# Kernel optimization log

Measured on AMD Instinct MI355X. Metric: run time of the kernel, lower is better.

## Reference

```python
import jax, jax.numpy as jnp
import numpy as np
from functools import partial

K = 64
KERNEL_SIZE = 16
TAU = 10.0
THETA = 0.5
GAMMA = 10.0
ALPHA = float(np.exp(-1.0 / TAU))
BETA = 1.0 - ALPHA

@jax.custom_vjp
def spike(x):
    return (x >= 0).astype(x.dtype)

def _spike_fwd(x):
    return spike(x), x

def _spike_bwd(x, g):
    surrogate = GAMMA * jnp.maximum(1.0 - GAMMA * jnp.abs(x), 0.0)
    return (g * surrogate,)

spike.defvjp(_spike_fwd, _spike_bwd)

def setup_inputs() -> dict:
    key = jax.random.key(0)
    k1, k2 = jax.random.split(key)
    B, T = 256, 4096
    x = jax.random.normal(k1, (B, 1, T), dtype=jnp.float32)
    # conv weight [K, 1, ks], init N(0, 1/sqrt(ks))
    W = jax.random.normal(k2, (K, 1, KERNEL_SIZE), dtype=jnp.float32) / np.sqrt(KERNEL_SIZE)
    return {"x": x, "W": W}

def _forward(x, W):
    B = x.shape[0]
    x = x.reshape(B, 1, -1)  # [B,1,T]
    # causal conv: left pad ks-1 -> output length T
    u = jax.lax.conv_general_dilated(
        x, W,
        window_strides=(1,),
        padding=[(KERNEL_SIZE - 1, 0)],
        dimension_numbers=("NCH", "OIH", "NCH"),
    )  # [B,K,T]
    u_t = jnp.transpose(u, (2, 0, 1))  # [T,B,K]
    v0 = jnp.zeros((B, K), dtype=x.dtype)

    def step(v, ut):
        v = ALPHA * v + BETA * ut                      # leak + input
        s_raw = spike(v - THETA)                        # [B,K]
        winner = jax.lax.stop_gradient(jnp.argmax(v, axis=1))  # [B]
        winner_spiked = jnp.take_along_axis(s_raw, winner[:, None], axis=1)  # [B,1]
        wta_mask = jax.nn.one_hot(winner, K, dtype=s_raw.dtype) * winner_spiked
        s = s_raw * wta_mask
        v = v - s * THETA                               # reset
        return v, s

    _, spikes_t = jax.lax.scan(step, v0, u_t)  # [T,B,K]
    return jnp.transpose(spikes_t, (1, 2, 0))  # [B,K,T]

def reference(x, W):
    return _forward(x, W)
```

## Files before the change

### kernel.cpp

```cpp
#include <hip/hip_runtime.h>

#define T_LEN  4096
#define KS     16
#define NSEG   8
#define SEG_CH 32
#define WARM_CH 24

#define ALPHA_F 0.9048374180359595f
#define BETA_F  0.09516258196404048f
#define THETA_F 0.5f

__device__ __forceinline__ float wave64_max_all(float v) {
  float m, t;
  asm("s_nop 1\n\t"
      "v_max_f32 %0, %2, %2 quad_perm:[1,0,3,2] row_mask:0xf bank_mask:0xf\n\t"
      "s_nop 1\n\t"
      "v_max_f32 %0, %0, %0 quad_perm:[2,3,0,1] row_mask:0xf bank_mask:0xf\n\t"
      "s_nop 1\n\t"
      "v_max_f32 %0, %0, %0 row_half_mirror row_mask:0xf bank_mask:0xf\n\t"
      "s_nop 1\n\t"
      "v_max_f32 %0, %0, %0 row_mirror row_mask:0xf bank_mask:0xf\n\t"
      "v_mov_b32 %1, %0\n\t"
      "s_nop 1\n\t"
      "v_permlane32_swap_b32 %1, %0\n\t"
      "s_nop 1\n\t"
      "v_max_f32 %0, %0, %1\n\t"
      "v_mov_b32 %1, %0\n\t"
      "s_nop 1\n\t"
      "v_permlane16_swap_b32 %1, %0\n\t"
      "s_nop 1\n\t"
      "v_max_f32 %0, %0, %1"
      : "=&v"(m), "=&v"(t)
      : "v"(v));
  return m;
}

__global__ __launch_bounds__(128, 4)
void convlif_wta_kernel(const float* __restrict__ x, const float* __restrict__ W,
                        float* __restrict__ out) {
  const int blk  = blockIdx.x;
  const int b    = blk >> 3;
  const int seg  = blk & (NSEG - 1);
  const int wave = threadIdx.x >> 6;
  const int lane = threadIdx.x & 63;

  const int cout0  = seg * SEG_CH;
  const int cstart = (cout0 > WARM_CH) ? (cout0 - WARM_CH) : 0;
  const int cend   = cout0 + SEG_CH;
  const int nch    = cend - cstart;

  __shared__ float vbuf[2][64];

  float w[KS];
  {
    const float4* w4 = reinterpret_cast<const float4*>(W + lane * KS);
    #pragma unroll
    for (int q = 0; q < 4; ++q) {
      float4 a = w4[q];
      w[4*q+0] = a.x; w[4*q+1] = a.y; w[4*q+2] = a.z; w[4*q+3] = a.w;
    }
  }

  const float4* xv4 = reinterpret_cast<const float4*>(x + (size_t)b * T_LEN);
  float* orow = out + ((size_t)(b * 64 + lane)) * T_LEN;

  float u[16];

  auto conv_chunk = [&](int c) {
    float xf[32];
    if (c == 0) {
      #pragma unroll
      for (int m = 0; m < 16; ++m) xf[m] = 0.0f;
    } else {
      const int b4 = 4 * c - 4;
      #pragma unroll
      for (int q = 0; q < 4; ++q) {
        float4 a = xv4[b4 + q];
        xf[4*q+0] = a.x; xf[4*q+1] = a.y; xf[4*q+2] = a.z; xf[4*q+3] = a.w;
      }
    }
    #pragma unroll
    for (int q = 0; q < 4; ++q) {
      float4 a = xv4[4*c + q];
      xf[16+4*q+0] = a.x; xf[16+4*q+1] = a.y;
      xf[16+4*q+2] = a.z; xf[16+4*q+3] = a.w;
    }
    #pragma unroll
    for (int i = 0; i < 16; ++i) {
      float acc = w[0] * xf[1 + i];
      #pragma unroll
      for (int j = 1; j < KS; ++j) acc = fmaf(w[j], xf[1 + i + j], acc);
      u[i] = BETA_F * acc;
    }
  };

  if (wave == 0) conv_chunk(cstart);

  for (int s = 0; s < nch; ++s) {
    const int c = cstart + s;
    if ((s & 1) == wave) {
      float v = (s == 0) ? 0.0f : vbuf[(s - 1) & 1][lane];
      float sv[16];
      #pragma unroll
      for (int i = 0; i < 16; ++i) {
        float vr = fmaf(ALPHA_F, v, u[i]);
        float vm = vr - THETA_F;
        unsigned long long sp = __ballot(vr >= THETA_F);
        bool c1 = (vr >= THETA_F);
        sv[i] = c1 ? 1.0f : 0.0f;
        v     = c1 ? vm : vr;
        if (__builtin_expect((sp & (sp - 1ull)) != 0ull, 0)) {
          float m = wave64_max_all(vr);
          unsigned long long eq = __ballot(vr == m);
          bool win = (lane == __builtin_ctzll(eq));
          sv[i] = win ? 1.0f : 0.0f;
          v     = win ? vm : vr;
        }
      }
      vbuf[s & 1][lane] = v;

      if (c >= cout0) {
        float4* p = reinterpret_cast<float4*>(orow + (size_t)c * 16);
        p[0] = make_float4(sv[0],  sv[1],  sv[2],  sv[3]);
        p[1] = make_float4(sv[4],  sv[5],  sv[6],  sv[7]);
        p[2] = make_float4(sv[8],  sv[9],  sv[10], sv[11]);
        p[3] = make_float4(sv[12], sv[13], sv[14], sv[15]);
      }
    } else {
      if (c + 1 < cend) conv_chunk(c + 1);
    }
    __syncthreads();
  }
}

extern "C" void kernel_launch(void* const* d_in, const int* in_sizes, int n_in,
                              void* d_out, int out_size, void* d_ws, size_t ws_size,
                              hipStream_t stream) {
  const float* x   = (const float*)d_in[0];
  const float* W   = (const float*)d_in[1];
  float*       out = (float*)d_out;
  convlif_wta_kernel<<<dim3(256 * NSEG), dim3(128), 0, stream>>>(x, W, out);
}
```

Before: 115.3 us.

## Split conv producer across two waves in a rotating three-wave pipeline

```diff
diff --git a/kernel.cpp b/kernel.cpp
--- a/kernel.cpp
+++ b/kernel.cpp
@@ -35,7 +35,7 @@
   return m;
 }
 
-__global__ __launch_bounds__(128, 4)
+__global__ __launch_bounds__(192, 6)
 void convlif_wta_kernel(const float* __restrict__ x, const float* __restrict__ W,
                         float* __restrict__ out) {
   const int blk  = blockIdx.x;
@@ -49,6 +49,7 @@
   const int cend   = cout0 + SEG_CH;
   const int nch    = cend - cstart;
 
+  __shared__ float uh_lds[2][8][64];
   __shared__ float vbuf[2][64];
 
   float w[KS];
@@ -64,46 +65,83 @@
   const float4* xv4 = reinterpret_cast<const float4*>(x + (size_t)b * T_LEN);
   float* orow = out + ((size_t)(b * 64 + lane)) * T_LEN;
 
-  float u[16];
+  float ulo[8];
 
-  auto conv_chunk = [&](int c) {
-    float xf[32];
-    if (c == 0) {
+  auto conv_lo = [&](int cc) {
+    float xf[24];
+    if (cc == 0) {
       #pragma unroll
       for (int m = 0; m < 16; ++m) xf[m] = 0.0f;
+      #pragma unroll
+      for (int q = 0; q < 2; ++q) {
+        float4 a = xv4[q];
+        xf[16+4*q+0] = a.x; xf[16+4*q+1] = a.y;
+        xf[16+4*q+2] = a.z; xf[16+4*q+3] = a.w;
+      }
     } else {
-      const int b4 = 4 * c - 4;
+      const int b4 = 4 * cc - 4;
       #pragma unroll
-      for (int q = 0; q < 4; ++q) {
+      for (int q = 0; q < 6; ++q) {
         float4 a = xv4[b4 + q];
         xf[4*q+0] = a.x; xf[4*q+1] = a.y; xf[4*q+2] = a.z; xf[4*q+3] = a.w;
       }
     }
     #pragma unroll
-    for (int q = 0; q < 4; ++q) {
-      float4 a = xv4[4*c + q];
-      xf[16+4*q+0] = a.x; xf[16+4*q+1] = a.y;
-      xf[16+4*q+2] = a.z; xf[16+4*q+3] = a.w;
-    }
-    #pragma unroll
-    for (int i = 0; i < 16; ++i) {
+    for (int i = 0; i < 8; ++i) {
       float acc = w[0] * xf[1 + i];
       #pragma unroll
       for (int j = 1; j < KS; ++j) acc = fmaf(w[j], xf[1 + i + j], acc);
-      u[i] = BETA_F * acc;
+      ulo[i] = BETA_F * acc;
     }
   };
 
-  if (wave == 0) conv_chunk(cstart);
+  auto conv_hi = [&](int cc, int slot) {
+    float xf[32];
+    if (cc == 0) {
+      #pragma unroll
+      for (int m = 8; m < 16; ++m) xf[m] = 0.0f;
+      #pragma unroll
+      for (int q = 0; q < 4; ++q) {
+        float4 a = xv4[q];
+        xf[16+4*q+0] = a.x; xf[16+4*q+1] = a.y;
+        xf[16+4*q+2] = a.z; xf[16+4*q+3] = a.w;
+      }
+    } else {
+      const int b4 = 4 * cc - 4;
+      #pragma unroll
+      for (int q = 2; q < 8; ++q) {
+        float4 a = xv4[b4 + q];
+        xf[4*q+0] = a.x; xf[4*q+1] = a.y; xf[4*q+2] = a.z; xf[4*q+3] = a.w;
+      }
+    }
+    #pragma unroll
+    for (int i = 8; i < 16; ++i) {
+      float acc = w[0] * xf[1 + i];
+      #pragma unroll
+      for (int j = 1; j < KS; ++j) acc = fmaf(w[j], xf[1 + i + j], acc);
+      uh_lds[slot][i - 8][lane] = BETA_F * acc;
+    }
+  };
+
+  if (wave == 0) conv_lo(cstart);
+  if (wave == 2) conv_hi(cstart, 0);
+  __syncthreads();
 
   for (int s = 0; s < nch; ++s) {
-    const int c = cstart + s;
-    if ((s & 1) == wave) {
+    const int c    = cstart + s;
+    const int role = s % 3;
+
+    if (wave == role) {
+      float uhi[8];
+      #pragma unroll
+      for (int q = 0; q < 8; ++q) uhi[q] = uh_lds[s & 1][q][lane];
       float v = (s == 0) ? 0.0f : vbuf[(s - 1) & 1][lane];
+
       float sv[16];
       #pragma unroll
       for (int i = 0; i < 16; ++i) {
-        float vr = fmaf(ALPHA_F, v, u[i]);
+        float ui = (i < 8) ? ulo[i] : uhi[i - 8];
+        float vr = fmaf(ALPHA_F, v, ui);
         float vm = vr - THETA_F;
         unsigned long long sp = __ballot(vr >= THETA_F);
         bool c1 = (vr >= THETA_F);
@@ -126,8 +164,10 @@
         p[2] = make_float4(sv[8],  sv[9],  sv[10], sv[11]);
         p[3] = make_float4(sv[12], sv[13], sv[14], sv[15]);
       }
+    } else if (wave == ((role + 1) % 3)) {
+      if (s + 1 < nch) conv_lo(c + 1);
     } else {
-      if (c + 1 < cend) conv_chunk(c + 1);
+      if (s + 1 < nch) conv_hi(c + 1, (s + 1) & 1);
     }
     __syncthreads();
   }
@@ -139,5 +179,5 @@
   const float* x   = (const float*)d_in[0];
   const float* W   = (const float*)d_in[1];
   float*       out = (float*)d_out;
-  convlif_wta_kernel<<<dim3(256 * NSEG), dim3(128), 0, stream>>>(x, W, out);
+  convlif_wta_kernel<<<dim3(256 * NSEG), dim3(192), 0, stream>>>(x, W, out);
 }
```

New measurement: 126.4 us. +9.6%, slower.

## Specialize waves into conv producer and LIF consumer via shared-memory double buffer

Applied to the files above, without the earlier changes.

```diff
diff --git a/kernel.cpp b/kernel.cpp
--- a/kernel.cpp
+++ b/kernel.cpp
@@ -5,6 +5,7 @@
 #define NSEG   8
 #define SEG_CH 32
 #define WARM_CH 24
+#define USTRIDE 18
 
 #define ALPHA_F 0.9048374180359595f
 #define BETA_F  0.09516258196404048f
@@ -47,89 +48,113 @@
   const int cout0  = seg * SEG_CH;
   const int cstart = (cout0 > WARM_CH) ? (cout0 - WARM_CH) : 0;
   const int cend   = cout0 + SEG_CH;
-  const int nch    = cend - cstart;
+  const int npair  = (cend - cstart) >> 1;
 
-  __shared__ float vbuf[2][64];
-
-  float w[KS];
-  {
-    const float4* w4 = reinterpret_cast<const float4*>(W + lane * KS);
-    #pragma unroll
-    for (int q = 0; q < 4; ++q) {
-      float4 a = w4[q];
-      w[4*q+0] = a.x; w[4*q+1] = a.y; w[4*q+2] = a.z; w[4*q+3] = a.w;
-    }
-  }
+  __shared__ float dbuf[2][2][64][USTRIDE];
 
   const float4* xv4 = reinterpret_cast<const float4*>(x + (size_t)b * T_LEN);
   float* orow = out + ((size_t)(b * 64 + lane)) * T_LEN;
 
-  float u[16];
-
-  auto conv_chunk = [&](int c) {
-    float xf[32];
-    if (c == 0) {
-      #pragma unroll
-      for (int m = 0; m < 16; ++m) xf[m] = 0.0f;
-    } else {
-      const int b4 = 4 * c - 4;
+  if (wave == 1) {
+    float w[KS];
+    {
+      const float4* w4 = reinterpret_cast<const float4*>(W + lane * KS);
       #pragma unroll
       for (int q = 0; q < 4; ++q) {
-        float4 a = xv4[b4 + q];
-        xf[4*q+0] = a.x; xf[4*q+1] = a.y; xf[4*q+2] = a.z; xf[4*q+3] = a.w;
+        float4 a = w4[q];
+        w[4*q+0] = a.x; w[4*q+1] = a.y; w[4*q+2] = a.z; w[4*q+3] = a.w;
       }
     }
-    #pragma unroll
-    for (int q = 0; q < 4; ++q) {
-      float4 a = xv4[4*c + q];
-      xf[16+4*q+0] = a.x; xf[16+4*q+1] = a.y;
-      xf[16+4*q+2] = a.z; xf[16+4*q+3] = a.w;
-    }
-    #pragma unroll
-    for (int i = 0; i < 16; ++i) {
-      float acc = w[0] * xf[1 + i];
-      #pragma unroll
-      for (int j = 1; j < KS; ++j) acc = fmaf(w[j], xf[1 + i + j], acc);
-      u[i] = BETA_F * acc;
-    }
-  };
 
-  if (wave == 0) conv_chunk(cstart);
+    for (int p = 0; p <= npair; ++p) {
+      if (p < npair) {
+        #pragma unroll
+        for (int ch = 0; ch < 2; ++ch) {
+          const int c = cstart + 2 * p + ch;
+          float xf[32];
+          if (c == 0) {
+            #pragma unroll
+            for (int m = 0; m < 16; ++m) xf[m] = 0.0f;
+          } else {
+            const int b4 = 4 * c - 4;
+            #pragma unroll
+            for (int q = 0; q < 4; ++q) {
+              float4 a = xv4[b4 + q];
+              xf[4*q+0] = a.x; xf[4*q+1] = a.y; xf[4*q+2] = a.z; xf[4*q+3] = a.w;
+            }
+          }
+          #pragma unroll
+          for (int q = 0; q < 4; ++q) {
+            float4 a = xv4[4*c + q];
+            xf[16+4*q+0] = a.x; xf[16+4*q+1] = a.y;
+            xf[16+4*q+2] = a.z; xf[16+4*q+3] = a.w;
+          }
 
-  for (int s = 0; s < nch; ++s) {
-    const int c = cstart + s;
-    if ((s & 1) == wave) {
-      float v = (s == 0) ? 0.0f : vbuf[(s - 1) & 1][lane];
-      float sv[16];
-      #pragma unroll
-      for (int i = 0; i < 16; ++i) {
-        float vr = fmaf(ALPHA_F, v, u[i]);
-        float vm = vr - THETA_F;
-        unsigned long long sp = __ballot(vr >= THETA_F);
-        bool c1 = (vr >= THETA_F);
-        sv[i] = c1 ? 1.0f : 0.0f;
-        v     = c1 ? vm : vr;
-        if (__builtin_expect((sp & (sp - 1ull)) != 0ull, 0)) {
-          float m = wave64_max_all(vr);
-          unsigned long long eq = __ballot(vr == m);
-          bool win = (lane == __builtin_ctzll(eq));
-          sv[i] = win ? 1.0f : 0.0f;
-          v     = win ? vm : vr;
+          float* ur = &dbuf[p & 1][ch][lane][0];
+          #pragma unroll
+          for (int i = 0; i < 16; i += 2) {
+            float acc0 = w[0] * xf[1 + i];
+            #pragma unroll
+            for (int j = 1; j < KS; ++j) acc0 = fmaf(w[j], xf[1 + i + j], acc0);
+            float acc1 = w[0] * xf[2 + i];
+            #pragma unroll
+            for (int j = 1; j < KS; ++j) acc1 = fmaf(w[j], xf[2 + i + j], acc1);
+            *reinterpret_cast<float2*>(ur + i) =
+                make_float2(BETA_F * acc0, BETA_F * acc1);
+          }
         }
       }
-      vbuf[s & 1][lane] = v;
+      __syncthreads();
+    }
+  } else {
+    float v = 0.0f;
 
-      if (c >= cout0) {
-        float4* p = reinterpret_cast<float4*>(orow + (size_t)c * 16);
-        p[0] = make_float4(sv[0],  sv[1],  sv[2],  sv[3]);
-        p[1] = make_float4(sv[4],  sv[5],  sv[6],  sv[7]);
-        p[2] = make_float4(sv[8],  sv[9],  sv[10], sv[11]);
-        p[3] = make_float4(sv[12], sv[13], sv[14], sv[15]);
+    for (int p = 0; p <= npair; ++p) {
+      if (p >= 1) {
+        const int slot = (p - 1) & 1;
+        #pragma unroll
+        for (int ch = 0; ch < 2; ++ch) {
+          const int c = cstart + 2 * (p - 1) + ch;
+
+          float u[16];
+          {
+            const float* ur = &dbuf[slot][ch][lane][0];
+            #pragma unroll
+            for (int i = 0; i < 16; i += 2) {
+              float2 t2 = *reinterpret_cast<const float2*>(ur + i);
+              u[i] = t2.x; u[i + 1] = t2.y;
+            }
+          }
+
+          float sv[16];
+          #pragma unroll
+          for (int i = 0; i < 16; ++i) {
+            float vr = fmaf(ALPHA_F, v, u[i]);
+            float vm = vr - THETA_F;
+            unsigned long long sp = __ballot(vr >= THETA_F);
+            bool c1 = (vr >= THETA_F);
+            sv[i] = c1 ? 1.0f : 0.0f;
+            v     = c1 ? vm : vr;
+            if (__builtin_expect((sp & (sp - 1ull)) != 0ull, 0)) {
+              float m = wave64_max_all(vr);
+              unsigned long long eq = __ballot(vr == m);
+              bool win = (lane == __builtin_ctzll(eq));
+              sv[i] = win ? 1.0f : 0.0f;
+              v     = win ? vm : vr;
+            }
+          }
+
+          if (c >= cout0) {
+            float4* pp = reinterpret_cast<float4*>(orow + (size_t)c * 16);
+            pp[0] = make_float4(sv[0],  sv[1],  sv[2],  sv[3]);
+            pp[1] = make_float4(sv[4],  sv[5],  sv[6],  sv[7]);
+            pp[2] = make_float4(sv[8],  sv[9],  sv[10], sv[11]);
+            pp[3] = make_float4(sv[12], sv[13], sv[14], sv[15]);
+          }
+        }
       }
-    } else {
-      if (c + 1 < cend) conv_chunk(c + 1);
+      __syncthreads();
     }
-    __syncthreads();
   }
 }
 
```

Measured after the change: 109.7 us. -4.8%, faster.
